# Kernel tuning notes

Measured on AMD Instinct MI355X. Metric: run time of the kernel, lower is better.

Reference implementation:

```python
import jax, jax.numpy as jnp
import numpy as np

B, N_VIS, N_HID1, N_HID2 = 1024, 4096, 4096, 4096


def setup_inputs() -> dict:
    key = jax.random.key(0)
    k0, k1, k2, k3 = jax.random.split(key, 4)
    v_data = (jax.random.uniform(k0, (B, N_VIS)) < 0.5).astype(jnp.float32)
    occupant_data = (jax.random.uniform(k1, (B, N_VIS // 2)) < 0.5).astype(jnp.float32)
    bw1 = float(np.sqrt(6.0 / (N_HID1 + N_VIS)))   # xavier_uniform
    bw2 = float(np.sqrt(6.0 / (N_HID1 + N_HID2)))
    W1 = jax.random.uniform(k2, (N_HID1, N_VIS), jnp.float32, -bw1, bw1)
    W2 = jax.random.uniform(k3, (N_HID1, N_HID2), jnp.float32, -bw2, bw2)
    return {
        "v_data": v_data,
        "occupant_data": occupant_data,
        "W1": W1,
        "b_v": jnp.zeros((N_VIS,), jnp.float32),
        "b_h1": jnp.zeros((N_HID1,), jnp.float32),
        "W2": W2,
        "b_h2": jnp.zeros((N_HID2,), jnp.float32),
        "k": 2,
    }


def reference(v_data, occupant_data, W1, b_v, b_h1, W2, b_h2, k):
    key = jax.random.key(42)
    Bn, n_vis = v_data.shape
    n_hid2 = b_h2.shape[0]
    dt = v_data.dtype

    def bern(kk, p):
        return (jax.random.uniform(kk, p.shape, p.dtype) < p).astype(p.dtype)

    # literal torch math (n_hid1 == n_hid2):
    # F.linear(v, W1, b_h1) + F.linear(h2, W2.T) = v@W1.T + b_h1 + h2@W2
    def p_h1(v, h2):
        return jax.nn.sigmoid(v @ W1.T + b_h1 + h2 @ W2)

    def p_h2(h1):  # F.linear(h1, W2, b_h2) = h1@W2.T + b_h2
        return jax.nn.sigmoid(h1 @ W2.T + b_h2)

    def p_v(h1):   # F.linear(h1, W1.T, b_v) = h1@W1 + b_v
        return jax.nn.sigmoid(h1 @ W1 + b_v)

    kpos1, kpos2, kfin, kloop = jax.random.split(key, 4)

    # positive phase (no_grad in torch)
    h2_zeros = jnp.zeros((Bn, n_hid2), dt)
    h1_data = bern(kpos1, jax.lax.stop_gradient(p_h1(v_data, h2_zeros)))
    h2_data = bern(kpos2, jax.lax.stop_gradient(p_h2(h1_data)))

    # negative phase: k Gibbs steps with occupant clamping
    v_neg, h2_neg = v_data, h2_data
    for i in range(k):
        ka, kb, kc = jax.random.split(jax.random.fold_in(kloop, i), 3)
        h1_neg = bern(ka, p_h1(v_neg, h2_neg))
        h2_neg = bern(kb, p_h2(h1_neg))
        pv = p_v(h1_neg)
        sign_s = bern(kc, pv[:, 1::2])
        # occupant_clamp: occupant bits from data, sign bits sampled
        v_neg = jnp.stack([occupant_data, sign_s], axis=-1).reshape(Bn, n_vis)

    h1_neg_final = bern(kfin, jax.lax.stop_gradient(p_h1(v_neg, h2_neg)))

    pos_v_sign = v_data[:, 1::2]
    neg_v_sign = v_neg[:, 1::2]
    invB = 1.0 / Bn

    # mean over batch of outer products == single matmul / B
    dW1_sign = (jnp.einsum('bi,bj->ij', pos_v_sign, h1_data)
                - jnp.einsum('bi,bj->ij', neg_v_sign, h1_neg_final)) * invB
    dW1_full = jnp.zeros_like(W1).at[:, 1::2].set(dW1_sign.T)
    db_v_full = jnp.zeros_like(b_v).at[1::2].set((pos_v_sign - neg_v_sign).mean(0))
    db_h1 = (h1_data - h1_neg_final).mean(0)
    dW2 = (jnp.einsum('bi,bj->ij', h1_data, h2_data)
           - jnp.einsum('bi,bj->ij', h1_neg_final, h2_neg)) * invB
    db_h2 = (h2_data - h2_neg).mean(0)

    eps = jnp.asarray(1e-7, dt)
    sp, st = v_neg[:, 1::2], v_data[:, 1::2]
    loss = -(st * jnp.log(sp + eps) + (1 - st) * jnp.log(1 - sp + eps)).mean()

    # torch sets p.grad = -dX; return loss plus those grads
    return (loss, -dW1_full, -db_v_full, -db_h1, -dW2, -db_h2)
```

## Files before the change

kernel.cpp:

```cpp
#include <hip/hip_runtime.h>
#include <stdint.h>
#include <math.h>

#define B_SZ 1024
#define NV   4096
#define NH   4096
#define NSGN 2048

typedef short bf16x8 __attribute__((ext_vector_type(8)));
typedef short bf16x4 __attribute__((ext_vector_type(4)));
typedef float f32x4  __attribute__((ext_vector_type(4)));
typedef _Float16 f16x8 __attribute__((ext_vector_type(8)));

#define F16_ONE  ((short)0x3C00)
#define F16_NEG1 ((short)0xBC00)

__host__ __device__ __forceinline__ void tf2x32(uint32_t k0, uint32_t k1,
                                                uint32_t x0, uint32_t x1,
                                                uint32_t& o0, uint32_t& o1)
{
    uint32_t k2 = k0 ^ k1 ^ 0x1BD11BDAu;
#define TFR(r) { x0 += x1; x1 = (x1 << (r)) | (x1 >> (32 - (r))); x1 ^= x0; }
    x0 += k0; x1 += k1;
    TFR(13) TFR(15) TFR(26) TFR(6)
    x0 += k1; x1 += k2 + 1u;
    TFR(17) TFR(29) TFR(16) TFR(24)
    x0 += k2; x1 += k0 + 2u;
    TFR(13) TFR(15) TFR(26) TFR(6)
    x0 += k0; x1 += k1 + 3u;
    TFR(17) TFR(29) TFR(16) TFR(24)
    x0 += k1; x1 += k2 + 4u;
    TFR(13) TFR(15) TFR(26) TFR(6)
    x0 += k2; x1 += k0 + 5u;
#undef TFR
    o0 = x0; o1 = x1;
}

__device__ __forceinline__ float tf_uniform01(uint32_t k0, uint32_t k1, uint32_t idx)
{
    uint32_t a, b;
    tf2x32(k0, k1, 0u, idx, a, b);
    uint32_t bits = a ^ b;
    uint32_t fb = (bits >> 9) | 0x3F800000u;
    return __uint_as_float(fb) - 1.0f;
}

__device__ __forceinline__ float sigmoidf_(float x)
{
    if (x >= 0.0f) { float e = expf(-x); return 1.0f / (1.0f + e); }
    float e = expf(x); return e / (1.0f + e);
}

__device__ __forceinline__ void gl16(const void* g, void* l)
{
    __builtin_amdgcn_global_load_lds((const __attribute__((address_space(1))) void*)g,
                                     (__attribute__((address_space(3))) void*)l, 16, 0, 0);
}

__global__ __launch_bounds__(256) void conv_tr(const float* __restrict__ W,
                                               short* __restrict__ Wf,
                                               short* __restrict__ Wt)
{
    __shared__ short t[64][65];
    const int bx = blockIdx.x * 64;
    const int by = blockIdx.y * 64;
    const int r0 = threadIdx.x >> 4;
    const int c0 = (threadIdx.x & 15) * 4;
#pragma unroll
    for (int i = 0; i < 4; ++i) {
        int row = by + r0 + i * 16;
        f32x4 v = *(const f32x4*)(W + (size_t)row * 4096 + bx + c0);
        short h[4];
#pragma unroll
        for (int j = 0; j < 4; ++j) {
            union { _Float16 f; short s; } u;
            u.f = (_Float16)v[j];
            h[j] = u.s;
        }
        *(bf16x4*)(Wf + (size_t)row * 4096 + bx + c0) = *(bf16x4*)h;
#pragma unroll
        for (int j = 0; j < 4; ++j) t[c0 + j][r0 + i * 16] = h[j];
    }
    __syncthreads();
#pragma unroll
    for (int i = 0; i < 4; ++i) {
        int orow = r0 + i * 16;
        short o[4] = { t[orow][c0], t[orow][c0 + 1], t[orow][c0 + 2], t[orow][c0 + 3] };
        *(bf16x4*)(Wt + (size_t)(bx + orow) * 4096 + by + c0) = *(bf16x4*)o;
    }
}

template<int NEG>
__global__ __launch_bounds__(256) void tr16(const short* __restrict__ in,
                                            short* __restrict__ out)
{
    __shared__ short t[64][65];
    const int bx = blockIdx.x * 64;
    const int by = blockIdx.y * 64;
    const int r0 = threadIdx.x >> 4;
    const int c0 = (threadIdx.x & 15) * 4;
#pragma unroll
    for (int i = 0; i < 4; ++i) {
        int row = by + r0 + i * 16;
        bf16x4 v = *(const bf16x4*)(in + (size_t)row * 4096 + bx + c0);
#pragma unroll
        for (int j = 0; j < 4; ++j)
            t[c0 + j][r0 + i * 16] = NEG ? (short)(v[j] ^ (short)0x8000) : v[j];
    }
    __syncthreads();
#pragma unroll
    for (int i = 0; i < 4; ++i) {
        int orow = r0 + i * 16;
        short o[4] = { t[orow][c0], t[orow][c0 + 1], t[orow][c0 + 2], t[orow][c0 + 3] };
        *(bf16x4*)(out + (size_t)(bx + orow) * 1024 + by + c0) = *(bf16x4*)o;
    }
}

__global__ __launch_bounds__(256) void tr_sign(const short* __restrict__ in,
                                               short* __restrict__ out)
{
    __shared__ short t[64][65];
    const int bx = blockIdx.x * 64;
    const int by = blockIdx.y * 64;
    const int r0 = threadIdx.x >> 4;
    const int c0 = (threadIdx.x & 15) * 4;
#pragma unroll
    for (int i = 0; i < 4; ++i) {
        int row = by + r0 + i * 16;
        bf16x8 v = *(const bf16x8*)(in + (size_t)row * 4096 + 2 * (bx + c0));
#pragma unroll
        for (int j = 0; j < 4; ++j) t[c0 + j][r0 + i * 16] = v[2 * j + 1];
    }
    __syncthreads();
#pragma unroll
    for (int i = 0; i < 4; ++i) {
        int orow = r0 + i * 16;
        short o[4] = { t[orow][c0], t[orow][c0 + 1], t[orow][c0 + 2], t[orow][c0 + 3] };
        *(bf16x4*)(out + (size_t)(bx + orow) * 1024 + by + c0) = *(bf16x4*)o;
    }
}

__global__ __launch_bounds__(256) void tr_signf(const float* __restrict__ in,
                                                short* __restrict__ out)
{
    __shared__ short t[64][65];
    const int bx = blockIdx.x * 64;
    const int by = blockIdx.y * 64;
    const int r0 = threadIdx.x >> 4;
    const int c0 = (threadIdx.x & 15) * 4;
#pragma unroll
    for (int i = 0; i < 4; ++i) {
        int row = by + r0 + i * 16;
        const float* p = in + (size_t)row * 4096 + 2 * (bx + c0);
        f32x4 a = *(const f32x4*)p;
        f32x4 b = *(const f32x4*)(p + 4);
        t[c0 + 0][r0 + i * 16] = (a[1] != 0.0f) ? F16_NEG1 : (short)0;
        t[c0 + 1][r0 + i * 16] = (a[3] != 0.0f) ? F16_NEG1 : (short)0;
        t[c0 + 2][r0 + i * 16] = (b[1] != 0.0f) ? F16_NEG1 : (short)0;
        t[c0 + 3][r0 + i * 16] = (b[3] != 0.0f) ? F16_NEG1 : (short)0;
    }
    __syncthreads();
#pragma unroll
    for (int i = 0; i < 4; ++i) {
        int orow = r0 + i * 16;
        short o[4] = { t[orow][c0], t[orow][c0 + 1], t[orow][c0 + 2], t[orow][c0 + 3] };
        *(bf16x4*)(out + (size_t)(bx + orow) * 1024 + by + c0) = *(bf16x4*)o;
    }
}

template<int MODE>
__global__ __launch_bounds__(512, 2) void mm_chunk(
    const short* __restrict__ A0, const short* __restrict__ A1,
    const short* __restrict__ B0, const short* __restrict__ B1,
    float* __restrict__ P)
{
    __shared__ __align__(1024) short As[2][16 * 512];
    __shared__ __align__(1024) short Bs[2][8 * 512];

    const int bid = blockIdx.x;
    const int xcd = bid & 7, slot = bid >> 3;

    int bm, bncol, ck, kbase, NW;
    const short* Ap;
    const short* Bp;
    if (MODE == 2) {
        int pn = xcd * 8 + (slot & 7);
        bm = ((slot >> 3) & 3) * 256;
        ck = slot >> 5;
        kbase = ck * 2048;
        Ap = A0;
        Bp = (pn < 32) ? (B0 + (size_t)pn * 128 * 4096)
                       : (B1 + (size_t)(pn - 32) * 128 * 4096);
        bncol = pn * 128;
        NW = 8192;
    } else {
        int pn = xcd * 4 + (slot & 3);
        bm = ((slot >> 2) & 3) * 256;
        ck = slot >> 4;
        if (MODE == 1) {
            if (ck >= 2) { Ap = A1; Bp = B1 + (size_t)pn * 128 * 4096; kbase = (ck - 2) * 2048; }
            else         { Ap = A0; Bp = B0 + (size_t)pn * 128 * 4096; kbase = ck * 2048; }
        } else {
            Ap = A0; Bp = B0 + (size_t)pn * 128 * 4096; kbase = ck * 1024;
        }
        bncol = pn * 128;
        NW = 4096;
    }

    const int NT = (MODE == 0) ? 32 : 64;

    const int tid = threadIdx.x;
    const int wv = tid >> 6, lane = tid & 63;
    const int l15 = lane & 15, l4 = lane >> 4;
    const int fr = l15, fc = l4 * 8;
    const int wm = wv >> 1, wn = wv & 1;

    f32x4 acc[4][4] = {};

    auto stage = [&](int buf, int t) {
        const int kk = kbase + t * 32;
        gl16(Ap + (size_t)(bm + (wv * 2 + 0) * 16 + fr) * 4096 + kk + fc, &As[buf][(wv * 2 + 0) * 512]);
        gl16(Ap + (size_t)(bm + (wv * 2 + 1) * 16 + fr) * 4096 + kk + fc, &As[buf][(wv * 2 + 1) * 512]);
        gl16(Bp + (size_t)(wv * 16 + fr) * 4096 + kk + fc, &Bs[buf][wv * 512]);
    };
    auto compute = [&](int buf) {
        f16x8 xf[4], yf[4];
#pragma unroll
        for (int m = 0; m < 4; ++m)
            xf[m] = *(f16x8*)&As[buf][(wm * 4 + m) * 512 + lane * 8];
#pragma unroll
        for (int n = 0; n < 4; ++n)
            yf[n] = *(f16x8*)&Bs[buf][(wn * 4 + n) * 512 + lane * 8];
#pragma unroll
        for (int m = 0; m < 4; ++m)
#pragma unroll
            for (int n = 0; n < 4; ++n)
                acc[m][n] = __builtin_amdgcn_mfma_f32_16x16x32_f16(xf[m], yf[n], acc[m][n], 0, 0, 0);
    };

    stage(0, 0);
    __syncthreads();
    for (int t = 0; t < NT; ++t) {
        const int cur = t & 1;
        if (t + 1 < NT) stage(cur ^ 1, t + 1);
        compute(cur);
        __syncthreads();
    }

    float* Pc = P + (size_t)ck * 1024 * NW;
#pragma unroll
    for (int m = 0; m < 4; ++m)
#pragma unroll
        for (int n = 0; n < 4; ++n)
#pragma unroll
            for (int r = 0; r < 4; ++r) {
                int row = bm + wm * 64 + m * 16 + l4 * 4 + r;
                int col = bncol + wn * 64 + n * 16 + l15;
                Pc[(size_t)row * NW + col] = acc[m][n][r];
            }
}

__global__ __launch_bounds__(512, 2) void grad2(
    const short* __restrict__ XnT, const short* __restrict__ YnT,
    const short* __restrict__ XpT, const short* __restrict__ YpT,
    float* __restrict__ Out)
{
    __shared__ __align__(1024) short As[2][16 * 512];
    __shared__ __align__(1024) short Bs[2][8 * 512];

    const int bid = blockIdx.x;
    const int xcd = bid & 7, slot = bid >> 3;
    const int pn = xcd * 4 + (slot & 3);
    const int bm = (slot >> 2) * 256;

    const int tid = threadIdx.x;
    const int wv = tid >> 6, lane = tid & 63;
    const int l15 = lane & 15, l4 = lane >> 4;
    const int fr = l15, fc = l4 * 8;
    const int wm = wv >> 1, wn = wv & 1;

    f32x4 acc[4][4] = {};

    auto stage = [&](int buf, int t) {
        const short* X = (t < 32) ? XnT : XpT;
        const short* Y = (t < 32) ? YnT : YpT;
        const int kk = (t & 31) * 32;
        gl16(X + (size_t)(bm + (wv * 2 + 0) * 16 + fr) * 1024 + kk + fc, &As[buf][(wv * 2 + 0) * 512]);
        gl16(X + (size_t)(bm + (wv * 2 + 1) * 16 + fr) * 1024 + kk + fc, &As[buf][(wv * 2 + 1) * 512]);
        gl16(Y + (size_t)(pn * 128 + wv * 16 + fr) * 1024 + kk + fc, &Bs[buf][wv * 512]);
    };
    auto compute = [&](int buf) {
        f16x8 xf[4], yf[4];
#pragma unroll
        for (int m = 0; m < 4; ++m)
            xf[m] = *(f16x8*)&As[buf][(wm * 4 + m) * 512 + lane * 8];
#pragma unroll
        for (int n = 0; n < 4; ++n)
            yf[n] = *(f16x8*)&Bs[buf][(wn * 4 + n) * 512 + lane * 8];
#pragma unroll
        for (int m = 0; m < 4; ++m)
#pragma unroll
            for (int n = 0; n < 4; ++n)
                acc[m][n] = __builtin_amdgcn_mfma_f32_16x16x32_f16(xf[m], yf[n], acc[m][n], 0, 0, 0);
    };

    stage(0, 0);
    __syncthreads();
    for (int t = 0; t < 64; ++t) {
        const int cur = t & 1;
        if (t + 1 < 64) stage(cur ^ 1, t + 1);
        compute(cur);
        __syncthreads();
    }

    const float invB = 1.0f / 1024.0f;
#pragma unroll
    for (int m = 0; m < 4; ++m)
#pragma unroll
        for (int n = 0; n < 4; ++n)
#pragma unroll
            for (int r = 0; r < 4; ++r) {
                int i_ = bm + wm * 64 + m * 16 + l4 * 4 + r;
                int j_ = pn * 128 + wn * 64 + n * 16 + l15;
                Out[(size_t)i_ * 4096 + j_] = acc[m][n][r] * invB;
            }
}

__global__ __launch_bounds__(256, 4) void grad1(
    const short* __restrict__ XnT, const short* __restrict__ YnT,
    const short* __restrict__ XpT, const short* __restrict__ YpT,
    float* __restrict__ Out)
{
    __shared__ __align__(1024) short As[2][8 * 512];
    __shared__ __align__(1024) short Bs[2][8 * 512];

    const int bid = blockIdx.x;
    const int xcd = bid & 7, slot = bid >> 3;
    const int pn = xcd * 2 + (slot & 1);
    const int bm = (slot >> 1) * 128;

    const int tid = threadIdx.x;
    const int wv = tid >> 6, lane = tid & 63;
    const int l15 = lane & 15, l4 = lane >> 4;
    const int fr = l15, fc = l4 * 8;
    const int wm = wv >> 1, wn = wv & 1;

    f32x4 acc[4][4] = {};

    auto stage = [&](int buf, int t) {
        const short* X = (t < 32) ? XnT : XpT;
        const short* Y = (t < 32) ? YnT : YpT;
        const int kk = (t & 31) * 32;
#pragma unroll
        for (int c = 0; c < 2; ++c) {
            int sub = wv * 2 + c;
            gl16(X + (size_t)(bm + sub * 16 + fr) * 1024 + kk + fc, &As[buf][sub * 512]);
            gl16(Y + (size_t)(pn * 128 + sub * 16 + fr) * 1024 + kk + fc, &Bs[buf][sub * 512]);
        }
    };
    auto compute = [&](int buf) {
        f16x8 xf[4], yf[4];
#pragma unroll
        for (int m = 0; m < 4; ++m)
            xf[m] = *(f16x8*)&As[buf][(wm * 4 + m) * 512 + lane * 8];
#pragma unroll
        for (int n = 0; n < 4; ++n)
            yf[n] = *(f16x8*)&Bs[buf][(wn * 4 + n) * 512 + lane * 8];
#pragma unroll
        for (int m = 0; m < 4; ++m)
#pragma unroll
            for (int n = 0; n < 4; ++n)
                acc[m][n] = __builtin_amdgcn_mfma_f32_16x16x32_f16(xf[m], yf[n], acc[m][n], 0, 0, 0);
    };

    stage(0, 0);
    __syncthreads();
    for (int t = 0; t < 64; ++t) {
        const int cur = t & 1;
        if (t + 1 < 64) stage(cur ^ 1, t + 1);
        compute(cur);
        __syncthreads();
    }

    const float invB = 1.0f / 1024.0f;
#pragma unroll
    for (int m = 0; m < 4; ++m)
#pragma unroll
        for (int n = 0; n < 4; ++n)
#pragma unroll
            for (int r = 0; r < 4; ++r) {
                int i_ = bm + wm * 64 + m * 16 + l4 * 4 + r;
                int j_ = pn * 128 + wn * 64 + n * 16 + l15;
                Out[(size_t)i_ * 4096 + 2 * j_ + 1] = acc[m][n][r] * invB;
                Out[(size_t)i_ * 4096 + 2 * j_]     = 0.0f;
            }
}

template<int EPI, int NC>
__global__ __launch_bounds__(256) void combine_h(
    const float* __restrict__ P, const float* __restrict__ bias,
    short* __restrict__ O0, short* __restrict__ O1,
    uint32_t k0, uint32_t k1)
{
    size_t e0 = ((size_t)blockIdx.x * 256 + threadIdx.x) * 8;
    f32x4 s0 = {}, s1 = {};
#pragma unroll
    for (int c = 0; c < NC; ++c) {
        const float* p = P + (size_t)c * 4194304 + e0;
        s0 += *(const f32x4*)p;
        s1 += *(const f32x4*)(p + 4);
    }
    int col = (int)(e0 & 4095);
    short o[8];
#pragma unroll
    for (int j = 0; j < 8; ++j) {
        float v = ((j < 4) ? s0[j] : s1[j - 4]) + bias[col + j];
        float pr = sigmoidf_(v);
        float u = tf_uniform01(k0, k1, (uint32_t)(e0 + j));
        o[j] = (u < pr) ? F16_ONE : (short)0;
    }
    *(bf16x8*)&O0[e0] = *(bf16x8*)o;
    if (EPI == 1) *(bf16x8*)&O1[e0] = *(bf16x8*)o;
}

__global__ __launch_bounds__(256) void combine_dual(
    const float* __restrict__ P,
    const float* __restrict__ b_h2, const float* __restrict__ b_v,
    const float* __restrict__ occ,
    short* __restrict__ h2n, short* __restrict__ vneg,
    uint32_t kb0, uint32_t kb1, uint32_t kc0, uint32_t kc1)
{
    size_t e0 = ((size_t)blockIdx.x * 256 + threadIdx.x) * 8;
    int row = (int)(e0 >> 13);
    int cl  = (int)(e0 & 8191);
    f32x4 s0 = {}, s1 = {};
#pragma unroll
    for (int c = 0; c < 2; ++c) {
        const float* p = P + (size_t)c * 8388608 + e0;
        s0 += *(const f32x4*)p;
        s1 += *(const f32x4*)(p + 4);
    }
    short o[8];
    if (cl < 4096) {
#pragma unroll
        for (int j = 0; j < 8; ++j) {
            float v = ((j < 4) ? s0[j] : s1[j - 4]) + b_h2[cl + j];
            float pr = sigmoidf_(v);
            size_t e = (size_t)row * 4096 + cl + j;
            float u = tf_uniform01(kb0, kb1, (uint32_t)e);
            o[j] = (u < pr) ? F16_ONE : (short)0;
        }
        *(bf16x8*)&h2n[(size_t)row * 4096 + cl] = *(bf16x8*)o;
    } else {
        int v0 = cl - 4096;
#pragma unroll
        for (int j = 0; j < 8; ++j) {
            int vcol = v0 + j;
            if (vcol & 1) {
                int s = (vcol - 1) >> 1;
                float v = ((j < 4) ? s0[j] : s1[j - 4]) + b_v[vcol];
                float pr = sigmoidf_(v);
                float u = tf_uniform01(kc0, kc1, (uint32_t)(row * 2048 + s));
                o[j] = (u < pr) ? F16_ONE : (short)0;
            } else {
                o[j] = (occ[(size_t)row * 2048 + (vcol >> 1)] != 0.0f) ? F16_ONE : (short)0;
            }
        }
        *(bf16x8*)&vneg[(size_t)row * 4096 + v0] = *(bf16x8*)o;
    }
}

__global__ void cvt_kernel(const float* __restrict__ in, short* __restrict__ out, int n)
{
    int e = blockIdx.x * 256 + threadIdx.x;
    if (e < n) out[e] = (in[e] != 0.0f) ? F16_ONE : (short)0;
}

__global__ void dbv_fast(const float* __restrict__ vdata, const short* __restrict__ vneg,
                         float* __restrict__ out)
{
    __shared__ float part[4][64];
    int c = threadIdx.x & 63, rg = threadIdx.x >> 6;
    int s = blockIdx.x * 64 + c;
    float acc = 0.0f;
    for (int b = rg; b < B_SZ; b += 4)
        acc += ((vneg[(size_t)b * NV + 2 * s + 1] != 0) ? 1.0f : 0.0f)
             - vdata[(size_t)b * NV + 2 * s + 1];
    part[rg][c] = acc;
    __syncthreads();
    if (rg == 0) {
        out[2 * s + 1] = (part[0][c] + part[1][c] + part[2][c] + part[3][c]) * (1.0f / 1024.0f);
        out[2 * s] = 0.0f;
    }
}

__global__ void dbh_fast(const short* __restrict__ Xp, const short* __restrict__ Xn,
                         float* __restrict__ out)
{
    __shared__ int part[4][64];
    int c = threadIdx.x & 63, rg = threadIdx.x >> 6;
    int j = blockIdx.x * 64 + c;
    int acc = 0;
    for (int b = rg; b < B_SZ; b += 4)
        acc += (int)(Xn[(size_t)b * NH + j] != 0) - (int)(Xp[(size_t)b * NH + j] != 0);
    part[rg][c] = acc;
    __syncthreads();
    if (rg == 0)
        out[j] = (float)(part[0][c] + part[1][c] + part[2][c] + part[3][c]) * (1.0f / 1024.0f);
}

__global__ void zero_kernel(unsigned* p) { *p = 0u; }

__global__ void loss_count2(const float* __restrict__ vdata,
                            const short* __restrict__ vneg, unsigned* cnt)
{
    __shared__ int part[4];
    int t = blockIdx.x * 256 + threadIdx.x;
    int local = 0;
#pragma unroll
    for (int it = 0; it < 8; ++it) {
        int e = t + it * 262144;
        int b = e >> 11, s = e & 2047;
        float st = vdata[(size_t)b * NV + 2 * s + 1];
        float sp = (vneg[(size_t)b * NV + 2 * s + 1] != 0) ? 1.0f : 0.0f;
        local += (st != sp) ? 1 : 0;
    }
#pragma unroll
    for (int off = 32; off; off >>= 1) local += __shfl_down(local, off, 64);
    if ((threadIdx.x & 63) == 0) part[threadIdx.x >> 6] = local;
    __syncthreads();
    if (threadIdx.x == 0)
        atomicAdd(cnt, (unsigned)(part[0] + part[1] + part[2] + part[3]));
}

__global__ void loss_final_kernel(const unsigned* cnt, float* out, float lp, float lm)
{
    float mis = (float)(*cnt);
    float mat = 2097152.0f - mis;
    out[0] = -((mat * lp + mis * lm) * (1.0f / 2097152.0f));
}

extern "C" void kernel_launch(void* const* d_in, const int* in_sizes, int n_in,
                              void* d_out, int out_size, void* d_ws, size_t ws_size,
                              hipStream_t stream)
{
    (void)in_sizes; (void)n_in; (void)out_size; (void)ws_size;
    const float* v_data = (const float*)d_in[0];
    const float* occ    = (const float*)d_in[1];
    const float* W1     = (const float*)d_in[2];
    const float* b_v    = (const float*)d_in[3];
    const float* b_h1   = (const float*)d_in[4];
    const float* W2     = (const float*)d_in[5];
    const float* b_h2   = (const float*)d_in[6];
    float* out = (float*)d_out;

    char* w = (char*)d_ws;
    short* vneg = (short*)w;
    short* h1d  = vneg + (size_t)B_SZ * NV;
    short* h2d  = h1d  + (size_t)B_SZ * NH;
    short* h1c  = h2d  + (size_t)B_SZ * NH;
    short* h2n  = h1c  + (size_t)B_SZ * NH;
    float* P    = (float*)(h2n + (size_t)B_SZ * NH);
    unsigned* cnt = (unsigned*)(P + (size_t)4 * 1024 * 4096);

    short* h1cT  = (short*)P;
    short* h1dT  = h1cT  + (size_t)4096 * 1024;
    short* h2nT  = h1dT  + (size_t)4096 * 1024;
    short* h2dTn = h2nT  + (size_t)4096 * 1024;
    short* vsT   = h2dTn + (size_t)4096 * 1024;
    short* vdsTn = vsT   + (size_t)2048 * 1024;

    short* W1f = (short*)(((uintptr_t)(out + 1) + 15) & ~(uintptr_t)15);
    short* W1T = W1f + (size_t)NH * NV;
    short* W2f = W1T + (size_t)NH * NV;
    short* W2T = W2f + (size_t)NH * NH;

    const uint32_t r0 = 0u, r1 = 42u;
    uint32_t kp1a, kp1b, kp2a, kp2b, kfa, kfb, kla, klb;
    tf2x32(r0, r1, 0u, 0u, kp1a, kp1b);
    tf2x32(r0, r1, 0u, 1u, kp2a, kp2b);
    tf2x32(r0, r1, 0u, 2u, kfa, kfb);
    tf2x32(r0, r1, 0u, 3u, kla, klb);
    uint32_t kaA[2], kaB[2], kbA[2], kbB[2], kcA[2], kcB[2];
    for (int i = 0; i < 2; ++i) {
        uint32_t fa, fb;
        tf2x32(kla, klb, 0u, (uint32_t)i, fa, fb);
        tf2x32(fa, fb, 0u, 0u, kaA[i], kaB[i]);
        tf2x32(fa, fb, 0u, 1u, kbA[i], kbB[i]);
        tf2x32(fa, fb, 0u, 2u, kcA[i], kcB[i]);
    }

    const int T = 256;
    const int NELEM = B_SZ * NH;
    dim3 gTr(64, 64);

    conv_tr<<<gTr, 256, 0, stream>>>(W1, W1f, W1T);
    conv_tr<<<gTr, 256, 0, stream>>>(W2, W2f, W2T);

    cvt_kernel<<<NELEM / T, T, 0, stream>>>(v_data, vneg, NELEM);

    mm_chunk<0><<<512, 512, 0, stream>>>(vneg, nullptr, W1f, nullptr, P);
    combine_h<0, 4><<<2048, 256, 0, stream>>>(P, b_h1, h1d, nullptr, kp1a, kp1b);
    mm_chunk<0><<<512, 512, 0, stream>>>(h1d, nullptr, W2f, nullptr, P);
    combine_h<1, 4><<<2048, 256, 0, stream>>>(P, b_h2, h2d, h2n, kp2a, kp2b);

    for (int i = 0; i < 2; ++i) {
        mm_chunk<1><<<512, 512, 0, stream>>>(vneg, h2n, W1f, W2T, P);
        combine_h<0, 4><<<2048, 256, 0, stream>>>(P, b_h1, h1c, nullptr, kaA[i], kaB[i]);
        mm_chunk<2><<<512, 512, 0, stream>>>(h1c, nullptr, W2f, W1T, P);
        combine_dual<<<4096, 256, 0, stream>>>(P, b_h2, b_v, occ, h2n, vneg,
                                               kbA[i], kbB[i], kcA[i], kcB[i]);
    }

    mm_chunk<1><<<512, 512, 0, stream>>>(vneg, h2n, W1f, W2T, P);
    combine_h<0, 4><<<2048, 256, 0, stream>>>(P, b_h1, h1c, nullptr, kfa, kfb);

    float* dW1o  = out + 1;
    float* dbvo  = dW1o + (size_t)NH * NV;
    float* dbh1o = dbvo + NV;
    float* dW2o  = dbh1o + NH;
    float* dbh2o = dW2o + (size_t)NH * NH;

    dim3 gT16(64, 16), gTS(32, 16);
    tr16<0><<<gT16, 256, 0, stream>>>(h1c, h1cT);
    tr16<0><<<gT16, 256, 0, stream>>>(h1d, h1dT);
    tr16<0><<<gT16, 256, 0, stream>>>(h2n, h2nT);
    tr16<1><<<gT16, 256, 0, stream>>>(h2d, h2dTn);
    tr_sign<<<gTS, 256, 0, stream>>>(vneg, vsT);
    tr_signf<<<gTS, 256, 0, stream>>>(v_data, vdsTn);

    grad1<<<512, 256, 0, stream>>>(h1cT, vsT, h1dT, vdsTn, dW1o);
    grad2<<<512, 512, 0, stream>>>(h1cT, h2nT, h1dT, h2dTn, dW2o);

    dbv_fast<<<NSGN / 64, T, 0, stream>>>(v_data, vneg, dbvo);
    dbh_fast<<<NH / 64, T, 0, stream>>>(h1d, h1c, dbh1o);
    dbh_fast<<<NH / 64, T, 0, stream>>>(h2d, h2n, dbh2o);

    zero_kernel<<<1, 1, 0, stream>>>(cnt);
    loss_count2<<<1024, T, 0, stream>>>(v_data, vneg, cnt);
    loss_final_kernel<<<1, 1, 0, stream>>>(cnt, out, logf(1.0f + 1e-7f), logf(1e-7f));
}
```

Measured before the change: 1.226 ms.

## Compute only odd visible columns in p_v and store fp16 partial sums

The visible-layer matmul now uses a transposed W1 holding only the odd (sign) columns, so the fused h2/v matmul shrinks from 8192 to 6144 output columns and uses 384 blocks instead of 512. The even columns were never used because occupant bits come from the data. Split-K partial results are also written as fp16 instead of fp32, halving partial-buffer traffic between the matmul and combine kernels. The fp16 partials lose precision before the sigmoid and Bernoulli threshold, which can flip sampled bits near the boundary.

```diff
diff --git a/kernel.cpp b/kernel.cpp
--- a/kernel.cpp
+++ b/kernel.cpp
@@ -14,6 +14,13 @@
 
 #define F16_ONE  ((short)0x3C00)
 #define F16_NEG1 ((short)0xBC00)
+
+__device__ __forceinline__ short f32_to_f16s(float f)
+{
+    union { _Float16 h; short s; } u;
+    u.h = (_Float16)f;
+    return u.s;
+}
 
 __host__ __device__ __forceinline__ void tf2x32(uint32_t k0, uint32_t k1,
                                                 uint32_t x0, uint32_t x1,
@@ -72,14 +79,49 @@
         f32x4 v = *(const f32x4*)(W + (size_t)row * 4096 + bx + c0);
         short h[4];
 #pragma unroll
-        for (int j = 0; j < 4; ++j) {
-            union { _Float16 f; short s; } u;
-            u.f = (_Float16)v[j];
-            h[j] = u.s;
-        }
+        for (int j = 0; j < 4; ++j) h[j] = f32_to_f16s(v[j]);
         *(bf16x4*)(Wf + (size_t)row * 4096 + bx + c0) = *(bf16x4*)h;
 #pragma unroll
         for (int j = 0; j < 4; ++j) t[c0 + j][r0 + i * 16] = h[j];
+    }
+    __syncthreads();
+#pragma unroll
+    for (int i = 0; i < 4; ++i) {
+        int orow = r0 + i * 16;
+        short o[4] = { t[orow][c0], t[orow][c0 + 1], t[orow][c0 + 2], t[orow][c0 + 3] };
+        *(bf16x4*)(Wt + (size_t)(bx + orow) * 4096 + by + c0) = *(bf16x4*)o;
+    }
+}
+
+__global__ __launch_bounds__(256) void conv_f16(const float* __restrict__ W,
+                                                short* __restrict__ Wf)
+{
+    size_t i = ((size_t)blockIdx.x * 256 + threadIdx.x) * 4;
+    f32x4 v = *(const f32x4*)(W + i);
+    short h[4];
+#pragma unroll
+    for (int c = 0; c < 4; ++c) h[c] = f32_to_f16s(v[c]);
+    *(bf16x4*)(Wf + i) = *(bf16x4*)h;
+}
+
+__global__ __launch_bounds__(256) void conv_trodd(const float* __restrict__ W,
+                                                  short* __restrict__ Wt)
+{
+    __shared__ short t[64][65];
+    const int bx = blockIdx.x * 64;
+    const int by = blockIdx.y * 64;
+    const int r0 = threadIdx.x >> 4;
+    const int c0 = (threadIdx.x & 15) * 4;
+#pragma unroll
+    for (int i = 0; i < 4; ++i) {
+        int row = by + r0 + i * 16;
+        const float* p = W + (size_t)row * 4096 + 2 * (bx + c0);
+        f32x4 a = *(const f32x4*)p;
+        f32x4 b = *(const f32x4*)(p + 4);
+        t[c0 + 0][r0 + i * 16] = f32_to_f16s(a[1]);
+        t[c0 + 1][r0 + i * 16] = f32_to_f16s(a[3]);
+        t[c0 + 2][r0 + i * 16] = f32_to_f16s(b[1]);
+        t[c0 + 3][r0 + i * 16] = f32_to_f16s(b[3]);
     }
     __syncthreads();
 #pragma unroll
@@ -172,7 +214,7 @@
 __global__ __launch_bounds__(512, 2) void mm_chunk(
     const short* __restrict__ A0, const short* __restrict__ A1,
     const short* __restrict__ B0, const short* __restrict__ B1,
-    float* __restrict__ P)
+    short* __restrict__ P)
 {
     __shared__ __align__(1024) short As[2][16 * 512];
     __shared__ __align__(1024) short Bs[2][8 * 512];
@@ -184,15 +226,16 @@
     const short* Ap;
     const short* Bp;
     if (MODE == 2) {
-        int pn = xcd * 8 + (slot & 7);
-        bm = ((slot >> 3) & 3) * 256;
-        ck = slot >> 5;
+        int slot6 = slot % 6, rest = slot / 6;
+        int pn = xcd * 6 + slot6;
+        bm = (rest & 3) * 256;
+        ck = rest >> 2;
         kbase = ck * 2048;
         Ap = A0;
         Bp = (pn < 32) ? (B0 + (size_t)pn * 128 * 4096)
                        : (B1 + (size_t)(pn - 32) * 128 * 4096);
         bncol = pn * 128;
-        NW = 8192;
+        NW = 6144;
     } else {
         int pn = xcd * 4 + (slot & 3);
         bm = ((slot >> 2) & 3) * 256;
@@ -247,7 +290,7 @@
         __syncthreads();
     }
 
-    float* Pc = P + (size_t)ck * 1024 * NW;
+    short* Pc = P + (size_t)ck * 1024 * NW;
 #pragma unroll
     for (int m = 0; m < 4; ++m)
 #pragma unroll
@@ -256,7 +299,7 @@
             for (int r = 0; r < 4; ++r) {
                 int row = bm + wm * 64 + m * 16 + l4 * 4 + r;
                 int col = bncol + wn * 64 + n * 16 + l15;
-                Pc[(size_t)row * NW + col] = acc[m][n][r];
+                Pc[(size_t)row * NW + col] = f32_to_f16s(acc[m][n][r]);
             }
 }
 
@@ -398,23 +441,23 @@
 
 template<int EPI, int NC>
 __global__ __launch_bounds__(256) void combine_h(
-    const float* __restrict__ P, const float* __restrict__ bias,
+    const short* __restrict__ P, const float* __restrict__ bias,
     short* __restrict__ O0, short* __restrict__ O1,
     uint32_t k0, uint32_t k1)
 {
     size_t e0 = ((size_t)blockIdx.x * 256 + threadIdx.x) * 8;
-    f32x4 s0 = {}, s1 = {};
+    float s[8] = {};
 #pragma unroll
     for (int c = 0; c < NC; ++c) {
-        const float* p = P + (size_t)c * 4194304 + e0;
-        s0 += *(const f32x4*)p;
-        s1 += *(const f32x4*)(p + 4);
+        f16x8 v = *(const f16x8*)(P + (size_t)c * 4194304 + e0);
+#pragma unroll
+        for (int j = 0; j < 8; ++j) s[j] += (float)v[j];
     }
     int col = (int)(e0 & 4095);
     short o[8];
 #pragma unroll
     for (int j = 0; j < 8; ++j) {
-        float v = ((j < 4) ? s0[j] : s1[j - 4]) + bias[col + j];
+        float v = s[j] + bias[col + j];
         float pr = sigmoidf_(v);
         float u = tf_uniform01(k0, k1, (uint32_t)(e0 + j));
         o[j] = (u < pr) ? F16_ONE : (short)0;
@@ -424,27 +467,27 @@
 }
 
 __global__ __launch_bounds__(256) void combine_dual(
-    const float* __restrict__ P,
+    const short* __restrict__ P,
     const float* __restrict__ b_h2, const float* __restrict__ b_v,
     const float* __restrict__ occ,
     short* __restrict__ h2n, short* __restrict__ vneg,
     uint32_t kb0, uint32_t kb1, uint32_t kc0, uint32_t kc1)
 {
-    size_t e0 = ((size_t)blockIdx.x * 256 + threadIdx.x) * 8;
-    int row = (int)(e0 >> 13);
-    int cl  = (int)(e0 & 8191);
-    f32x4 s0 = {}, s1 = {};
+    int idx = blockIdx.x * 256 + threadIdx.x;
+    int row = idx / 768;
+    int cl  = (idx - row * 768) * 8;
+    float s[8] = {};
 #pragma unroll
     for (int c = 0; c < 2; ++c) {
-        const float* p = P + (size_t)c * 8388608 + e0;
-        s0 += *(const f32x4*)p;
-        s1 += *(const f32x4*)(p + 4);
-    }
-    short o[8];
+        f16x8 v = *(const f16x8*)(P + (size_t)c * 6291456 + (size_t)row * 6144 + cl);
+#pragma unroll
+        for (int j = 0; j < 8; ++j) s[j] += (float)v[j];
+    }
     if (cl < 4096) {
+        short o[8];
 #pragma unroll
         for (int j = 0; j < 8; ++j) {
-            float v = ((j < 4) ? s0[j] : s1[j - 4]) + b_h2[cl + j];
+            float v = s[j] + b_h2[cl + j];
             float pr = sigmoidf_(v);
             size_t e = (size_t)row * 4096 + cl + j;
             float u = tf_uniform01(kb0, kb1, (uint32_t)e);
@@ -452,21 +495,19 @@
         }
         *(bf16x8*)&h2n[(size_t)row * 4096 + cl] = *(bf16x8*)o;
     } else {
-        int v0 = cl - 4096;
+        int s0 = cl - 4096;
+        short o[16];
 #pragma unroll
         for (int j = 0; j < 8; ++j) {
-            int vcol = v0 + j;
-            if (vcol & 1) {
-                int s = (vcol - 1) >> 1;
-                float v = ((j < 4) ? s0[j] : s1[j - 4]) + b_v[vcol];
-                float pr = sigmoidf_(v);
-                float u = tf_uniform01(kc0, kc1, (uint32_t)(row * 2048 + s));
-                o[j] = (u < pr) ? F16_ONE : (short)0;
-            } else {
-                o[j] = (occ[(size_t)row * 2048 + (vcol >> 1)] != 0.0f) ? F16_ONE : (short)0;
-            }
+            int si = s0 + j;
+            float v = s[j] + b_v[2 * si + 1];
+            float pr = sigmoidf_(v);
+            float u = tf_uniform01(kc0, kc1, (uint32_t)(row * 2048 + si));
+            o[2 * j]     = (occ[(size_t)row * 2048 + si] != 0.0f) ? F16_ONE : (short)0;
+            o[2 * j + 1] = (u < pr) ? F16_ONE : (short)0;
         }
-        *(bf16x8*)&vneg[(size_t)row * 4096 + v0] = *(bf16x8*)o;
+        *(bf16x8*)&vneg[(size_t)row * 4096 + 2 * s0]     = *(bf16x8*)&o[0];
+        *(bf16x8*)&vneg[(size_t)row * 4096 + 2 * s0 + 8] = *(bf16x8*)&o[8];
     }
 }
 
@@ -560,20 +601,20 @@
     short* h2d  = h1d  + (size_t)B_SZ * NH;
     short* h1c  = h2d  + (size_t)B_SZ * NH;
     short* h2n  = h1c  + (size_t)B_SZ * NH;
-    float* P    = (float*)(h2n + (size_t)B_SZ * NH);
-    unsigned* cnt = (unsigned*)(P + (size_t)4 * 1024 * 4096);
-
-    short* h1cT  = (short*)P;
+    short* P    = h2n + (size_t)B_SZ * NH;
+    unsigned* cnt = (unsigned*)(P + (size_t)20 * 1024 * 1024);
+
+    short* h1cT  = P;
     short* h1dT  = h1cT  + (size_t)4096 * 1024;
     short* h2nT  = h1dT  + (size_t)4096 * 1024;
     short* h2dTn = h2nT  + (size_t)4096 * 1024;
     short* vsT   = h2dTn + (size_t)4096 * 1024;
     short* vdsTn = vsT   + (size_t)2048 * 1024;
 
-    short* W1f = (short*)(((uintptr_t)(out + 1) + 15) & ~(uintptr_t)15);
-    short* W1T = W1f + (size_t)NH * NV;
-    short* W2f = W1T + (size_t)NH * NV;
-    short* W2T = W2f + (size_t)NH * NH;
+    short* W1f  = (short*)(((uintptr_t)(out + 1) + 15) & ~(uintptr_t)15);
+    short* W1To = W1f  + (size_t)NH * NV;
+    short* W2f  = W1To + (size_t)NSGN * NV;
+    short* W2T  = W2f  + (size_t)NH * NH;
 
     const uint32_t r0 = 0u, r1 = 42u;
     uint32_t kp1a, kp1b, kp2a, kp2b, kfa, kfb, kla, klb;
@@ -592,10 +633,10 @@
 
     const int T = 256;
     const int NELEM = B_SZ * NH;
-    dim3 gTr(64, 64);
-
-    conv_tr<<<gTr, 256, 0, stream>>>(W1, W1f, W1T);
-    conv_tr<<<gTr, 256, 0, stream>>>(W2, W2f, W2T);
+
+    conv_f16<<<(NH * NV) / (4 * 256), 256, 0, stream>>>(W1, W1f);
+    conv_trodd<<<dim3(32, 64), 256, 0, stream>>>(W1, W1To);
+    conv_tr<<<dim3(64, 64), 256, 0, stream>>>(W2, W2f, W2T);
 
     cvt_kernel<<<NELEM / T, T, 0, stream>>>(v_data, vneg, NELEM);
 
@@ -607,8 +648,8 @@
     for (int i = 0; i < 2; ++i) {
         mm_chunk<1><<<512, 512, 0, stream>>>(vneg, h2n, W1f, W2T, P);
         combine_h<0, 4><<<2048, 256, 0, stream>>>(P, b_h1, h1c, nullptr, kaA[i], kaB[i]);
-        mm_chunk<2><<<512, 512, 0, stream>>>(h1c, nullptr, W2f, W1T, P);
-        combine_dual<<<4096, 256, 0, stream>>>(P, b_h2, b_v, occ, h2n, vneg,
+        mm_chunk<2><<<384, 512, 0, stream>>>(h1c, nullptr, W2f, W1To, P);
+        combine_dual<<<3072, 256, 0, stream>>>(P, b_h2, b_v, occ, h2n, vneg,
                                                kbA[i], kbB[i], kcA[i], kcB[i]);
     }
 
```

Measured after the change: 1.183 ms. -3.5%, faster.
